# Optimization experiments

Hardware: AMD Instinct MI355X
Metric: run time of the kernel (lower is better)

The kernel has to match this reference:

```python
import jax, jax.numpy as jnp
import numpy as np

NUM_CLUSTERS = 512
EMBED_DIM = 256
BATCH = 65536
ALPHA = 0.05

def setup_inputs() -> dict:
    key = jax.random.key(0)
    k1, k2 = jax.random.split(key)
    embeddings = jax.random.normal(k1, (BATCH, EMBED_DIM), dtype=jnp.float32)
    # torch.randn centers drawn inside forward; materialized here for determinism
    centers = jax.random.normal(k2, (NUM_CLUSTERS, EMBED_DIM), dtype=jnp.float32)
    return {"embeddings": embeddings, "centers": centers}

def reference(embeddings, centers):
    # the broadcast difference, without the huge [N, K, D] intermediate).
    x_sq = jnp.sum(embeddings * embeddings, axis=1, keepdims=True)      # [N, 1]
    c_sq = jnp.sum(centers * centers, axis=1)[None, :]                  # [1, K]
    cross = embeddings @ centers.T                                      # [N, K]
    distances = jnp.sqrt(jnp.maximum(x_sq + c_sq - 2.0 * cross, 0.0))   # [N, K]
    cluster_assignments = jnp.argmin(distances, axis=1)                 # [N] int
    # gather distance to assigned (nearest) center
    cluster_loss = jnp.take_along_axis(
        distances, cluster_assignments[:, None], axis=1)[:, 0]          # [N]
    kmeans_loss = jnp.mean(cluster_loss)
    return kmeans_loss * ALPHA
```

## Files before the change

### kernel.cpp

```cpp
#include <hip/hip_runtime.h>
#include <hip/hip_bf16.h>

#define NROWS 65536
#define DIM   256
#define KC    512
#define ALPHA 0.05f

#define BM   64
#define BN   64
#define SLD  264

typedef __attribute__((ext_vector_type(8))) short bf16x8;
typedef __attribute__((ext_vector_type(4))) float f32x4;

static __device__ __forceinline__ unsigned short f2bf(float f) {
    union { __hip_bfloat16 h; unsigned short u; } c;
    c.h = __float2bfloat16(f);
    return c.u;
}
static __device__ __forceinline__ float bf2f(unsigned short u) {
    union { unsigned short u; __hip_bfloat16 h; } c;
    c.u = u;
    return __bfloat162float(c.h);
}

__global__ void prep_centers(const float* __restrict__ centers,
                             float* __restrict__ c_sq,
                             unsigned short* __restrict__ cbf) {
    const int b = blockIdx.x;
    const int lane = threadIdx.x;
    const float4 v = reinterpret_cast<const float4*>(centers + (size_t)b * DIM)[lane];
    float s = v.x * v.x + v.y * v.y + v.z * v.z + v.w * v.w;
    ushort4 o;
    o.x = f2bf(v.x); o.y = f2bf(v.y); o.z = f2bf(v.z); o.w = f2bf(v.w);
    reinterpret_cast<ushort4*>(cbf + (size_t)b * DIM)[lane] = o;
    #pragma unroll
    for (int off = 32; off; off >>= 1) s += __shfl_xor(s, off, 64);
    if (lane == 0) c_sq[b] = s;
}

__global__ __launch_bounds__(256, 2) void kmeans_main(
    const float* __restrict__ emb,
    const unsigned short* __restrict__ cbf,
    const float* __restrict__ csq_g,
    float* __restrict__ out) {
    __shared__ unsigned short sA[BM * SLD];
    __shared__ unsigned short sB[BN * SLD];
    __shared__ float csq_s[KC];
    __shared__ float xsq_s[BM];
    __shared__ float rowmin_s[4][BM];

    const int t = threadIdx.x;
    const int w = t >> 6;
    const int lane = t & 63;
    const int m = lane & 15;
    const int q = lane >> 4;
    const int row0 = blockIdx.x * BM;

    const float4* embv = reinterpret_cast<const float4*>(emb + (size_t)row0 * DIM);
    #pragma unroll
    for (int i = 0; i < 16; ++i) {
        int f = t + 256 * i;
        int r = f >> 6;
        int c4 = f & 63;
        float4 v = embv[r * 64 + c4];
        ushort4 o;
        o.x = f2bf(v.x); o.y = f2bf(v.y); o.z = f2bf(v.z); o.w = f2bf(v.w);
        *reinterpret_cast<ushort4*>(&sA[r * SLD + c4 * 4]) = o;
    }
    csq_s[t] = csq_g[t];
    csq_s[t + 256] = csq_g[t + 256];
    __syncthreads();

    {
        int r = w * 16 + (lane >> 2);
        int qq = lane & 3;
        const ushort4* p = reinterpret_cast<const ushort4*>(&sA[r * SLD + qq * 64]);
        float s = 0.f;
        #pragma unroll
        for (int j = 0; j < 16; ++j) {
            ushort4 u = p[j];
            float a = bf2f(u.x), b = bf2f(u.y), c = bf2f(u.z), d = bf2f(u.w);
            s += a * a + b * b + c * c + d * d;
        }
        s += __shfl_xor(s, 1, 64);
        s += __shfl_xor(s, 2, 64);
        if (qq == 0) xsq_s[r] = s;
    }
    __syncthreads();

    bf16x8 afr[4][8];
    #pragma unroll
    for (int rt = 0; rt < 4; ++rt)
        #pragma unroll
        for (int k = 0; k < 8; ++k)
            afr[rt][k] = *reinterpret_cast<const bf16x8*>(
                &sA[(rt * 16 + m) * SLD + k * 32 + q * 8]);

    float minv[4][4];
    #pragma unroll
    for (int rt = 0; rt < 4; ++rt)
        #pragma unroll
        for (int rg = 0; rg < 4; ++rg) minv[rt][rg] = 1e30f;

    const uint4* cb4 = reinterpret_cast<const uint4*>(cbf);
    for (int ch = 0; ch < 8; ++ch) {
        #pragma unroll
        for (int i = 0; i < 8; ++i) {
            int f = t + 256 * i;
            int r = f >> 5;
            int c8 = f & 31;
            uint4 v = cb4[(size_t)(ch * BN + r) * 32 + c8];
            *reinterpret_cast<uint4*>(&sB[r * SLD + c8 * 8]) = v;
        }
        __syncthreads();

        bf16x8 bf[8];
        #pragma unroll
        for (int k = 0; k < 8; ++k)
            bf[k] = *reinterpret_cast<const bf16x8*>(
                &sB[(w * 16 + m) * SLD + k * 32 + q * 8]);

        const int col = ch * 64 + w * 16 + m;
        const float c2 = csq_s[col];
        #pragma unroll
        for (int rt = 0; rt < 4; ++rt) {
            f32x4 acc = {0.f, 0.f, 0.f, 0.f};
            #pragma unroll
            for (int k = 0; k < 8; ++k)
                acc = __builtin_amdgcn_mfma_f32_16x16x32_bf16(afr[rt][k], bf[k], acc, 0, 0, 0);
            #pragma unroll
            for (int rg = 0; rg < 4; ++rg) {
                float x2 = xsq_s[rt * 16 + q * 4 + rg];
                float d2 = x2 + c2 - 2.f * acc[rg];
                minv[rt][rg] = fminf(minv[rt][rg], d2);
            }
        }
        __syncthreads();
    }

    #pragma unroll
    for (int rt = 0; rt < 4; ++rt)
        #pragma unroll
        for (int rg = 0; rg < 4; ++rg) {
            float v = minv[rt][rg];
            v = fminf(v, __shfl_xor(v, 1, 64));
            v = fminf(v, __shfl_xor(v, 2, 64));
            v = fminf(v, __shfl_xor(v, 4, 64));
            v = fminf(v, __shfl_xor(v, 8, 64));
            if (m == 0) rowmin_s[w][rt * 16 + q * 4 + rg] = v;
        }
    __syncthreads();

    if (t < 64) {
        float v = fminf(fminf(rowmin_s[0][t], rowmin_s[1][t]),
                        fminf(rowmin_s[2][t], rowmin_s[3][t]));
        float d = sqrtf(fmaxf(v, 0.f));
        #pragma unroll
        for (int off = 1; off < 64; off <<= 1) d += __shfl_xor(d, off, 64);
        if (t == 0) atomicAdd(out, d * (ALPHA / (float)NROWS));
    }
}

extern "C" void kernel_launch(void* const* d_in, const int* in_sizes, int n_in,
                              void* d_out, int out_size, void* d_ws, size_t ws_size,
                              hipStream_t stream) {
    const float* emb     = (const float*)d_in[0];
    const float* centers = (const float*)d_in[1];
    float* out = (float*)d_out;

    float* c_sq = (float*)d_ws;
    unsigned short* cbf = (unsigned short*)((char*)d_ws + 2048);

    hipMemsetAsync(d_out, 0, sizeof(float), stream);
    prep_centers<<<dim3(KC), dim3(64), 0, stream>>>(centers, c_sq, cbf);
    kmeans_main<<<dim3(NROWS / BM), dim3(256), 0, stream>>>(emb, cbf, c_sq, out);
}
```

Before: 122.0 us.

## Pre-swizzle centers into MFMA fragment layout and load B directly to registers

The prep kernel now writes the bf16 centers in the exact per-lane MFMA fragment order and stores half the squared norms. The main kernel drops the shared-memory B tile and its per-chunk barriers, loads B fragments straight from global memory with next-chunk prefetch into registers, and folds -0.5*||c||^2 into the accumulator init so it tracks a max of x·c - 0.5||c||^2. The row norm is added back only once per row at the end. The output memset moves into the prep kernel, removing one launch. Register pressure goes up from double-buffered B fragments, and every wave reads B from global/L2 instead of sharing it through LDS.

```diff
diff --git a/kernel.cpp b/kernel.cpp
--- a/kernel.cpp
+++ b/kernel.cpp
@@ -7,7 +7,6 @@
 #define ALPHA 0.05f
 
 #define BM   64
-#define BN   64
 #define SLD  264
 
 typedef __attribute__((ext_vector_type(8))) short bf16x8;
@@ -25,30 +24,37 @@
 }
 
 __global__ void prep_centers(const float* __restrict__ centers,
-                             float* __restrict__ c_sq,
-                             unsigned short* __restrict__ cbf) {
-    const int b = blockIdx.x;
-    const int lane = threadIdx.x;
-    const float4 v = reinterpret_cast<const float4*>(centers + (size_t)b * DIM)[lane];
-    float s = v.x * v.x + v.y * v.y + v.z * v.z + v.w * v.w;
-    ushort4 o;
-    o.x = f2bf(v.x); o.y = f2bf(v.y); o.z = f2bf(v.z); o.w = f2bf(v.w);
-    reinterpret_cast<ushort4*>(cbf + (size_t)b * DIM)[lane] = o;
+                             float* __restrict__ csqh,
+                             uint4* __restrict__ cbf2,
+                             float* __restrict__ out) {
+    const int t = threadIdx.x;
+    const int r = blockIdx.x * 8 + (t >> 5);
+    const int e = t & 31;
+    const float4* cv = reinterpret_cast<const float4*>(centers);
+    float4 v0 = cv[r * 64 + e * 2];
+    float4 v1 = cv[r * 64 + e * 2 + 1];
+    float s = v0.x * v0.x + v0.y * v0.y + v0.z * v0.z + v0.w * v0.w
+            + v1.x * v1.x + v1.y * v1.y + v1.z * v1.z + v1.w * v1.w;
+    unsigned short o[8];
+    o[0] = f2bf(v0.x); o[1] = f2bf(v0.y); o[2] = f2bf(v0.z); o[3] = f2bf(v0.w);
+    o[4] = f2bf(v1.x); o[5] = f2bf(v1.y); o[6] = f2bf(v1.z); o[7] = f2bf(v1.w);
+    const int ch = r >> 6, w = (r >> 4) & 3, m = r & 15;
+    const int kk = e >> 2, q = e & 3, l = q * 16 + m;
+    cbf2[(((ch * 4 + w) * 8) + kk) * 64 + l] = *reinterpret_cast<uint4*>(o);
     #pragma unroll
-    for (int off = 32; off; off >>= 1) s += __shfl_xor(s, off, 64);
-    if (lane == 0) c_sq[b] = s;
+    for (int off = 16; off; off >>= 1) s += __shfl_xor(s, off, 64);
+    if (e == 0) csqh[r] = 0.5f * s;
+    if (blockIdx.x == 0 && t == 0) out[0] = 0.f;
 }
 
 __global__ __launch_bounds__(256, 2) void kmeans_main(
     const float* __restrict__ emb,
-    const unsigned short* __restrict__ cbf,
-    const float* __restrict__ csq_g,
+    const uint4* __restrict__ cbf2,
+    const float* __restrict__ csqh_g,
     float* __restrict__ out) {
     __shared__ unsigned short sA[BM * SLD];
-    __shared__ unsigned short sB[BN * SLD];
-    __shared__ float csq_s[KC];
     __shared__ float xsq_s[BM];
-    __shared__ float rowmin_s[4][BM];
+    __shared__ float rowmax_s[4][BM];
 
     const int t = threadIdx.x;
     const int w = t >> 6;
@@ -68,8 +74,6 @@
         o.x = f2bf(v.x); o.y = f2bf(v.y); o.z = f2bf(v.z); o.w = f2bf(v.w);
         *reinterpret_cast<ushort4*>(&sA[r * SLD + c4 * 4]) = o;
     }
-    csq_s[t] = csq_g[t];
-    csq_s[t + 256] = csq_g[t + 256];
     __syncthreads();
 
     {
@@ -87,7 +91,6 @@
         s += __shfl_xor(s, 2, 64);
         if (qq == 0) xsq_s[r] = s;
     }
-    __syncthreads();
 
     bf16x8 afr[4][8];
     #pragma unroll
@@ -97,65 +100,69 @@
             afr[rt][k] = *reinterpret_cast<const bf16x8*>(
                 &sA[(rt * 16 + m) * SLD + k * 32 + q * 8]);
 
-    float minv[4][4];
+    float c2h[8];
+    #pragma unroll
+    for (int ch = 0; ch < 8; ++ch) c2h[ch] = csqh_g[ch * 64 + w * 16 + m];
+
+    float maxv[4][4];
     #pragma unroll
     for (int rt = 0; rt < 4; ++rt)
         #pragma unroll
-        for (int rg = 0; rg < 4; ++rg) minv[rt][rg] = 1e30f;
+        for (int rg = 0; rg < 4; ++rg) maxv[rt][rg] = -1e30f;
 
-    const uint4* cb4 = reinterpret_cast<const uint4*>(cbf);
+    const bf16x8* cb2 = reinterpret_cast<const bf16x8*>(cbf2);
+
+    bf16x8 bcur[8];
+    #pragma unroll
+    for (int kk = 0; kk < 8; ++kk)
+        bcur[kk] = cb2[((0 * 4 + w) * 8 + kk) * 64 + lane];
+
+    #pragma unroll
     for (int ch = 0; ch < 8; ++ch) {
+        bf16x8 bnxt[8];
+        if (ch < 7) {
+            #pragma unroll
+            for (int kk = 0; kk < 8; ++kk)
+                bnxt[kk] = cb2[(((ch + 1) * 4 + w) * 8 + kk) * 64 + lane];
+        }
+        const float ci = -c2h[ch];
+        f32x4 acc[4];
         #pragma unroll
-        for (int i = 0; i < 8; ++i) {
-            int f = t + 256 * i;
-            int r = f >> 5;
-            int c8 = f & 31;
-            uint4 v = cb4[(size_t)(ch * BN + r) * 32 + c8];
-            *reinterpret_cast<uint4*>(&sB[r * SLD + c8 * 8]) = v;
+        for (int rt = 0; rt < 4; ++rt) acc[rt] = (f32x4){ci, ci, ci, ci};
+        #pragma unroll
+        for (int kk = 0; kk < 8; ++kk)
+            #pragma unroll
+            for (int rt = 0; rt < 4; ++rt)
+                acc[rt] = __builtin_amdgcn_mfma_f32_16x16x32_bf16(
+                    afr[rt][kk], bcur[kk], acc[rt], 0, 0, 0);
+        #pragma unroll
+        for (int rt = 0; rt < 4; ++rt)
+            #pragma unroll
+            for (int rg = 0; rg < 4; ++rg)
+                maxv[rt][rg] = fmaxf(maxv[rt][rg], acc[rt][rg]);
+        if (ch < 7) {
+            #pragma unroll
+            for (int kk = 0; kk < 8; ++kk) bcur[kk] = bnxt[kk];
         }
-        __syncthreads();
-
-        bf16x8 bf[8];
-        #pragma unroll
-        for (int k = 0; k < 8; ++k)
-            bf[k] = *reinterpret_cast<const bf16x8*>(
-                &sB[(w * 16 + m) * SLD + k * 32 + q * 8]);
-
-        const int col = ch * 64 + w * 16 + m;
-        const float c2 = csq_s[col];
-        #pragma unroll
-        for (int rt = 0; rt < 4; ++rt) {
-            f32x4 acc = {0.f, 0.f, 0.f, 0.f};
-            #pragma unroll
-            for (int k = 0; k < 8; ++k)
-                acc = __builtin_amdgcn_mfma_f32_16x16x32_bf16(afr[rt][k], bf[k], acc, 0, 0, 0);
-            #pragma unroll
-            for (int rg = 0; rg < 4; ++rg) {
-                float x2 = xsq_s[rt * 16 + q * 4 + rg];
-                float d2 = x2 + c2 - 2.f * acc[rg];
-                minv[rt][rg] = fminf(minv[rt][rg], d2);
-            }
-        }
-        __syncthreads();
     }
 
     #pragma unroll
     for (int rt = 0; rt < 4; ++rt)
         #pragma unroll
         for (int rg = 0; rg < 4; ++rg) {
-            float v = minv[rt][rg];
-            v = fminf(v, __shfl_xor(v, 1, 64));
-            v = fminf(v, __shfl_xor(v, 2, 64));
-            v = fminf(v, __shfl_xor(v, 4, 64));
-            v = fminf(v, __shfl_xor(v, 8, 64));
-            if (m == 0) rowmin_s[w][rt * 16 + q * 4 + rg] = v;
+            float v = maxv[rt][rg];
+            v = fmaxf(v, __shfl_xor(v, 1, 64));
+            v = fmaxf(v, __shfl_xor(v, 2, 64));
+            v = fmaxf(v, __shfl_xor(v, 4, 64));
+            v = fmaxf(v, __shfl_xor(v, 8, 64));
+            if (m == 0) rowmax_s[w][rt * 16 + q * 4 + rg] = v;
         }
     __syncthreads();
 
     if (t < 64) {
-        float v = fminf(fminf(rowmin_s[0][t], rowmin_s[1][t]),
-                        fminf(rowmin_s[2][t], rowmin_s[3][t]));
-        float d = sqrtf(fmaxf(v, 0.f));
+        float M = fmaxf(fmaxf(rowmax_s[0][t], rowmax_s[1][t]),
+                        fmaxf(rowmax_s[2][t], rowmax_s[3][t]));
+        float d = sqrtf(fmaxf(xsq_s[t] - 2.f * M, 0.f));
         #pragma unroll
         for (int off = 1; off < 64; off <<= 1) d += __shfl_xor(d, off, 64);
         if (t == 0) atomicAdd(out, d * (ALPHA / (float)NROWS));
@@ -169,10 +176,9 @@
     const float* centers = (const float*)d_in[1];
     float* out = (float*)d_out;
 
-    float* c_sq = (float*)d_ws;
-    unsigned short* cbf = (unsigned short*)((char*)d_ws + 2048);
+    float* csqh = (float*)d_ws;
+    uint4* cbf2 = (uint4*)((char*)d_ws + 2048);
 
-    hipMemsetAsync(d_out, 0, sizeof(float), stream);
-    prep_centers<<<dim3(KC), dim3(64), 0, stream>>>(centers, c_sq, cbf);
-    kmeans_main<<<dim3(NROWS / BM), dim3(256), 0, stream>>>(emb, cbf, c_sq, out);
+    prep_centers<<<dim3(KC / 8), dim3(256), 0, stream>>>(centers, csqh, cbf2, out);
+    kmeans_main<<<dim3(NROWS / BM), dim3(256), 0, stream>>>(emb, cbf2, csqh, out);
 }
```

Result: faster. 118.7 us (-2.7%).
